# Performance work log

Measured on AMD Instinct MI355X. Metric: run time of the kernel, lower is better.

The kernel has to match this reference:

```python
import jax, jax.numpy as jnp
import numpy as np

CIN = 128
COUT = 128
B = 8192
N_DIAG = 17
LENS = [9 - abs(i - 8) for i in range(N_DIAG)]  # [1,2,...,9,...,2,1]


def setup_inputs() -> dict:
    key = jax.random.key(0)
    ks = jax.random.split(key, 2 + N_DIAG)
    d = {
        "weights": jax.random.normal(ks[0], (N_DIAG, COUT, CIN), jnp.float32),
        "bias": jax.random.normal(ks[1], (N_DIAG, COUT), jnp.float32),
    }
    for i, L in enumerate(LENS):
        d[f"x{i}"] = jax.random.normal(ks[2 + i], (B, L, CIN), jnp.float32)
    return d


def _diag_idx(i):
    # board positions (r, c) on anti-diagonal r + c == i of a 9x9 board
    rs = np.arange(max(0, i - 8), min(8, i) + 1)
    cs = i - rs
    return rs, cs


def _forward(weights, bias, xs):
    b = xs[0].shape[0]
    out = jnp.zeros((b, 9, 9, weights.shape[1]), xs[0].dtype)
    for i, x in enumerate(xs):
        # per-diagonal linear transform: (B, L_i, Cin) @ (Cout, Cin)^T + bias
        y = jnp.einsum('blc,oc->blo', x, weights[i]) + bias[i]
        rs, cs = _diag_idx(i)  # static numpy indices -> jit-friendly scatter
        out = out.at[:, rs, cs, :].set(y)
    return out


def reference(weights, bias, x0, x1, x2, x3, x4, x5, x6, x7, x8, x9, x10, x11,
              x12, x13, x14, x15, x16):
    xs = (x0, x1, x2, x3, x4, x5, x6, x7, x8, x9, x10, x11, x12, x13, x14,
          x15, x16)
    return _forward(weights, bias, xs)
```

## Files before the change

### kernel.cpp

```cpp
#include <hip/hip_runtime.h>
#include <hip/hip_bf16.h>

#define CIN 128
#define COUT 128

typedef __attribute__((ext_vector_type(8))) short short8;
typedef __attribute__((ext_vector_type(4))) float f32x4;

struct XPtrs { const float* p[17]; };

__device__ __forceinline__ unsigned short f2bf(float f) {
  unsigned u = __float_as_uint(f);
  return (unsigned short)((u + 0x7fffu + ((u >> 16) & 1u)) >> 16);
}

__global__ __launch_bounds__(256) void diag_linear_kernel(
    XPtrs xp, const float* __restrict__ W, const float* __restrict__ bias,
    float* __restrict__ out) {
  const int p = blockIdx.y;
  const int r = p / 9, c = p % 9;
  const int diag = r + c;
  const int start = (diag > 8) ? (diag - 8) : 0;
  const int l = r - start;
  const int L = 9 - ((diag > 8) ? (diag - 8) : (8 - diag));
  const float* __restrict__ x = xp.p[diag];

  const int btile = blockIdx.x;
  const int t = threadIdx.x;
  const int lane = t & 63;
  const int wave = t >> 6;
  const int lr = lane & 15;
  const int lg = lane >> 4;

  __shared__ short wlds[4][4][128][8];

  {
    const int n = t & 127;
    const int kh = t >> 7;
    const float* wrow = W + (size_t)diag * (COUT * CIN) + (size_t)n * CIN + kh * 64;
#pragma unroll
    for (int it = 0; it < 16; ++it) {
      const int k = kh * 64 + it * 4;
      float4 w4 = *(const float4*)(wrow + it * 4);
      const int s = k >> 5;
      const int g = (k >> 3) & 3;
      const int j0 = k & 7;
      unsigned u0 = (unsigned)f2bf(w4.x) | ((unsigned)f2bf(w4.y) << 16);
      unsigned u1 = (unsigned)f2bf(w4.z) | ((unsigned)f2bf(w4.w) << 16);
      *(uint2*)&wlds[s][g][n][j0] = make_uint2(u0, u1);
    }
  }

  short8 afrag[2][4];
#pragma unroll
  for (int mb = 0; mb < 2; ++mb) {
    const int brow = btile * 128 + wave * 32 + mb * 16 + lr;
    const float* xr = x + ((size_t)brow * L + l) * CIN;
#pragma unroll
    for (int s = 0; s < 4; ++s) {
      float4 a0 = *(const float4*)(xr + s * 32 + lg * 8);
      float4 a1 = *(const float4*)(xr + s * 32 + lg * 8 + 4);
      short8 f;
      f[0] = (short)f2bf(a0.x); f[1] = (short)f2bf(a0.y);
      f[2] = (short)f2bf(a0.z); f[3] = (short)f2bf(a0.w);
      f[4] = (short)f2bf(a1.x); f[5] = (short)f2bf(a1.y);
      f[6] = (short)f2bf(a1.z); f[7] = (short)f2bf(a1.w);
      afrag[mb][s] = f;
    }
  }

  float bfr[8];
#pragma unroll
  for (int nb = 0; nb < 8; ++nb)
    bfr[nb] = bias[diag * COUT + nb * 16 + lr];

  f32x4 acc[2][8];
#pragma unroll
  for (int mb = 0; mb < 2; ++mb)
#pragma unroll
    for (int nb = 0; nb < 8; ++nb)
      acc[mb][nb] = (f32x4){0.f, 0.f, 0.f, 0.f};

  __syncthreads();

#pragma unroll
  for (int nb = 0; nb < 8; ++nb) {
#pragma unroll
    for (int s = 0; s < 4; ++s) {
      short8 bfrag = *(const short8*)&wlds[s][lg][nb * 16 + lr][0];
      acc[0][nb] = __builtin_amdgcn_mfma_f32_16x16x32_bf16(afrag[0][s], bfrag, acc[0][nb], 0, 0, 0);
      acc[1][nb] = __builtin_amdgcn_mfma_f32_16x16x32_bf16(afrag[1][s], bfrag, acc[1][nb], 0, 0, 0);
    }
  }

#pragma unroll
  for (int mb = 0; mb < 2; ++mb) {
#pragma unroll
    for (int v = 0; v < 4; ++v) {
      const size_t b = (size_t)btile * 128 + wave * 32 + mb * 16 + lg * 4 + v;
      float* orow = out + (b * 81 + p) * 128;
#pragma unroll
      for (int nb = 0; nb < 8; ++nb)
        orow[nb * 16 + lr] = acc[mb][nb][v] + bfr[nb];
    }
  }
}

extern "C" void kernel_launch(void* const* d_in, const int* in_sizes, int n_in,
                              void* d_out, int out_size, void* d_ws, size_t ws_size,
                              hipStream_t stream) {
  const float* W = (const float*)d_in[0];
  const float* bias = (const float*)d_in[1];
  XPtrs xp;
  for (int i = 0; i < 17; ++i) xp.p[i] = (const float*)d_in[2 + i];
  float* out = (float*)d_out;
  dim3 grid(64, 81);
  diag_linear_kernel<<<grid, dim3(256), 0, stream>>>(xp, W, bias, out);
}
```

Before: 179.0 us.

## Pre-convert weights to bf16, flatten per-diagonal rows, swap MFMA operands for vector stores

```diff
diff --git a/kernel.cpp b/kernel.cpp
--- a/kernel.cpp
+++ b/kernel.cpp
@@ -1,8 +1,5 @@
 #include <hip/hip_runtime.h>
 #include <hip/hip_bf16.h>
-
-#define CIN 128
-#define COUT 128
 
 typedef __attribute__((ext_vector_type(8))) short short8;
 typedef __attribute__((ext_vector_type(4))) float f32x4;
@@ -14,94 +11,116 @@
   return (unsigned short)((u + 0x7fffu + ((u >> 16) & 1u)) >> 16);
 }
 
-__global__ __launch_bounds__(256) void diag_linear_kernel(
-    XPtrs xp, const float* __restrict__ W, const float* __restrict__ bias,
-    float* __restrict__ out) {
-  const int p = blockIdx.y;
-  const int r = p / 9, c = p % 9;
-  const int diag = r + c;
-  const int start = (diag > 8) ? (diag - 8) : 0;
-  const int l = r - start;
-  const int L = 9 - ((diag > 8) ? (diag - 8) : (8 - diag));
-  const float* __restrict__ x = xp.p[diag];
+__global__ __launch_bounds__(1024) void convert_w_kernel(
+    const float* __restrict__ W, unsigned short* __restrict__ ws) {
+  const int tid = blockIdx.x * 1024 + threadIdx.x;
+  const int d  = tid >> 11;
+  const int s2 = tid & 2047;
+  const int sg = s2 >> 7;
+  const int n  = s2 & 127;
+  const float* src = W + ((size_t)d * 128 + n) * 128 + sg * 8;
+  float4 a = *(const float4*)(src);
+  float4 b = *(const float4*)(src + 4);
+  unsigned u0 = (unsigned)f2bf(a.x) | ((unsigned)f2bf(a.y) << 16);
+  unsigned u1 = (unsigned)f2bf(a.z) | ((unsigned)f2bf(a.w) << 16);
+  unsigned u2 = (unsigned)f2bf(b.x) | ((unsigned)f2bf(b.y) << 16);
+  unsigned u3 = (unsigned)f2bf(b.z) | ((unsigned)f2bf(b.w) << 16);
+  uint4 v = make_uint4(u0, u1, u2, u3);
+  *(uint4*)(ws + (size_t)tid * 8) = v;
+}
 
-  const int btile = blockIdx.x;
+__global__ __launch_bounds__(256, 4) void diag_linear_kernel(
+    XPtrs xp, const unsigned short* __restrict__ wsrc,
+    const float* __restrict__ bias, float* __restrict__ out) {
+  int bid = blockIdx.x;
+  int d = 0, base = 0;
+  for (int i = 0; i < 17; ++i) {
+    int Li = 9 - ((i < 8) ? (8 - i) : (i - 8));
+    int nb = 32 * Li;
+    if (bid < base + nb) { d = i; break; }
+    base += nb;
+  }
+  const int chunk = bid - base;
+  const int L = 9 - ((d < 8) ? (8 - d) : (d - 8));
+  const int start = (d > 8) ? (d - 8) : 0;
+  const float* __restrict__ x = xp.p[d];
+
   const int t = threadIdx.x;
   const int lane = t & 63;
   const int wave = t >> 6;
   const int lr = lane & 15;
   const int lg = lane >> 4;
 
-  __shared__ short wlds[4][4][128][8];
+  __shared__ unsigned short wlds[2048 * 8];
 
   {
-    const int n = t & 127;
-    const int kh = t >> 7;
-    const float* wrow = W + (size_t)diag * (COUT * CIN) + (size_t)n * CIN + kh * 64;
+    const unsigned short* gw = wsrc + (size_t)d * 16384;
+    typedef const __attribute__((address_space(1))) unsigned int* gas_u32;
+    typedef __attribute__((address_space(3))) unsigned int* las_u32;
 #pragma unroll
-    for (int it = 0; it < 16; ++it) {
-      const int k = kh * 64 + it * 4;
-      float4 w4 = *(const float4*)(wrow + it * 4);
-      const int s = k >> 5;
-      const int g = (k >> 3) & 3;
-      const int j0 = k & 7;
-      unsigned u0 = (unsigned)f2bf(w4.x) | ((unsigned)f2bf(w4.y) << 16);
-      unsigned u1 = (unsigned)f2bf(w4.z) | ((unsigned)f2bf(w4.w) << 16);
-      *(uint2*)&wlds[s][g][n][j0] = make_uint2(u0, u1);
+    for (int i = 0; i < 8; ++i) {
+      const int slotbase = (wave * 8 + i) * 64;
+      __builtin_amdgcn_global_load_lds(
+          (gas_u32)(const void*)(gw + (size_t)(slotbase + lane) * 8),
+          (las_u32)(void*)(wlds + (size_t)slotbase * 8),
+          16, 0, 0);
     }
   }
 
-  short8 afrag[2][4];
-#pragma unroll
-  for (int mb = 0; mb < 2; ++mb) {
-    const int brow = btile * 128 + wave * 32 + mb * 16 + lr;
-    const float* xr = x + ((size_t)brow * L + l) * CIN;
-#pragma unroll
-    for (int s = 0; s < 4; ++s) {
-      float4 a0 = *(const float4*)(xr + s * 32 + lg * 8);
-      float4 a1 = *(const float4*)(xr + s * 32 + lg * 8 + 4);
-      short8 f;
-      f[0] = (short)f2bf(a0.x); f[1] = (short)f2bf(a0.y);
-      f[2] = (short)f2bf(a0.z); f[3] = (short)f2bf(a0.w);
-      f[4] = (short)f2bf(a1.x); f[5] = (short)f2bf(a1.y);
-      f[6] = (short)f2bf(a1.z); f[7] = (short)f2bf(a1.w);
-      afrag[mb][s] = f;
-    }
-  }
-
-  float bfr[8];
-#pragma unroll
-  for (int nb = 0; nb < 8; ++nb)
-    bfr[nb] = bias[diag * COUT + nb * 16 + lr];
-
-  f32x4 acc[2][8];
-#pragma unroll
-  for (int mb = 0; mb < 2; ++mb)
-#pragma unroll
-    for (int nb = 0; nb < 8; ++nb)
-      acc[mb][nb] = (f32x4){0.f, 0.f, 0.f, 0.f};
-
+  const int m0 = chunk * 256;
   __syncthreads();
 
 #pragma unroll
-  for (int nb = 0; nb < 8; ++nb) {
+  for (int sub = 0; sub < 2; ++sub) {
+    const int m0s = m0 + sub * 128 + wave * 32;
+
+    short8 xf[2][4];
+#pragma unroll
+    for (int mb = 0; mb < 2; ++mb) {
+      const float* xr = x + (size_t)(m0s + mb * 16 + lr) * 128;
+#pragma unroll
+      for (int s = 0; s < 4; ++s) {
+        float4 a0 = *(const float4*)(xr + s * 32 + lg * 8);
+        float4 a1 = *(const float4*)(xr + s * 32 + lg * 8 + 4);
+        short8 f;
+        f[0] = (short)f2bf(a0.x); f[1] = (short)f2bf(a0.y);
+        f[2] = (short)f2bf(a0.z); f[3] = (short)f2bf(a0.w);
+        f[4] = (short)f2bf(a1.x); f[5] = (short)f2bf(a1.y);
+        f[6] = (short)f2bf(a1.z); f[7] = (short)f2bf(a1.w);
+        xf[mb][s] = f;
+      }
+    }
+
+    f32x4 acc[8][2];
+#pragma unroll
+    for (int nb = 0; nb < 8; ++nb) {
+      acc[nb][0] = (f32x4){0.f, 0.f, 0.f, 0.f};
+      acc[nb][1] = (f32x4){0.f, 0.f, 0.f, 0.f};
+    }
+
 #pragma unroll
     for (int s = 0; s < 4; ++s) {
-      short8 bfrag = *(const short8*)&wlds[s][lg][nb * 16 + lr][0];
-      acc[0][nb] = __builtin_amdgcn_mfma_f32_16x16x32_bf16(afrag[0][s], bfrag, acc[0][nb], 0, 0, 0);
-      acc[1][nb] = __builtin_amdgcn_mfma_f32_16x16x32_bf16(afrag[1][s], bfrag, acc[1][nb], 0, 0, 0);
+#pragma unroll
+      for (int nb = 0; nb < 8; ++nb) {
+        short8 wf = *(const short8*)&wlds[(size_t)((s * 4 + lg) * 128 + nb * 16 + lr) * 8];
+        acc[nb][0] = __builtin_amdgcn_mfma_f32_16x16x32_bf16(wf, xf[0][s], acc[nb][0], 0, 0, 0);
+        acc[nb][1] = __builtin_amdgcn_mfma_f32_16x16x32_bf16(wf, xf[1][s], acc[nb][1], 0, 0, 0);
+      }
     }
-  }
 
 #pragma unroll
-  for (int mb = 0; mb < 2; ++mb) {
+    for (int mb = 0; mb < 2; ++mb) {
+      const int f = m0s + mb * 16 + lr;
+      const unsigned b = (unsigned)f / (unsigned)L;
+      const int l = f - (int)b * L;
+      float* orow = out + (size_t)b * 10368 + (size_t)(start * 8 + d) * 128
+                    + (size_t)l * 1024 + lg * 4;
 #pragma unroll
-    for (int v = 0; v < 4; ++v) {
-      const size_t b = (size_t)btile * 128 + wave * 32 + mb * 16 + lg * 4 + v;
-      float* orow = out + (b * 81 + p) * 128;
-#pragma unroll
-      for (int nb = 0; nb < 8; ++nb)
-        orow[nb * 16 + lr] = acc[mb][nb][v] + bfr[nb];
+      for (int nb = 0; nb < 8; ++nb) {
+        f32x4 bv = *(const f32x4*)(bias + d * 128 + nb * 16 + lg * 4);
+        f32x4 v = acc[nb][mb] + bv;
+        __builtin_nontemporal_store(v, (f32x4*)(orow + nb * 16));
+      }
     }
   }
 }
@@ -114,6 +133,8 @@
   XPtrs xp;
   for (int i = 0; i < 17; ++i) xp.p[i] = (const float*)d_in[2 + i];
   float* out = (float*)d_out;
-  dim3 grid(64, 81);
-  diag_linear_kernel<<<grid, dim3(256), 0, stream>>>(xp, W, bias, out);
+  unsigned short* ws = (unsigned short*)d_ws;
+
+  convert_w_kernel<<<34, 1024, 0, stream>>>(W, ws);
+  diag_linear_kernel<<<2592, 256, 0, stream>>>(xp, ws, bias, out);
 }
```

Measured after the change: 188.3 us. +5.2%, slower.
